# Kernel optimization log

Hardware: AMD Instinct MI355X
Metric: run time of the kernel (lower is better)

Reference implementation:

```python
import jax, jax.numpy as jnp
import numpy as np

TEMPERATURE = 0.1
GAMMA = 0.5
LOSS_WEIGHT = 1.0
N, D = 8192, 64
EPS_COS = 1e-8
EPS_NCE = 1e-6
SQ_EPS = 1e-12  # (1e-6 distance)^2


def setup_inputs() -> dict:
    key = jax.random.key(0)
    k1, k2, k3 = jax.random.split(key, 3)
    features = jax.random.normal(k1, (N, D), dtype=jnp.float32)
    labels = jax.random.randint(k2, (N,), 0, 3, dtype=jnp.int64)
    coords = jax.random.uniform(k3, (N, 3), dtype=jnp.float32)
    return {"features": features, "labels": labels, "coords": coords}


def reference(features, labels, coords):
    # line-point mask (label == 2); pairwise math on the masked subset is
    # expressed as full pairwise + (m_i & m_j) masking, mathematically
    # identical to extract-then-pairwise in the torch original.
    m = labels == 2                       # [N] bool
    mf = m.astype(features.dtype)
    L = jnp.sum(mf)                       # number of line points

    # cosine similarity: normalize then GEMM (== F.cosine_similarity pairwise)
    norm = jnp.maximum(jnp.linalg.norm(features, axis=1, keepdims=True), EPS_COS)
    fn = features / norm
    feat_sim = fn @ fn.T                  # [N, N]

    # squared pairwise coordinate distances (cdist^2), clamped >= 0
    sq_norm = jnp.sum(coords * coords, axis=1)
    sq = sq_norm[:, None] + sq_norm[None, :] - 2.0 * (coords @ coords.T)
    sq = jnp.maximum(sq, 0.0)             # [N, N]

    pair = m[:, None] & m[None, :]
    within = (sq < 1.0) & (sq > SQ_EPS)   # dist < 1.0 and dist > 1e-6
    pos = pair & within
    neg = pair & ~within                  # original neg_mask = ~pos over subset

    posf = pos.astype(feat_sim.dtype)
    negf = neg.astype(feat_sim.dtype)

    exp_sim = jnp.exp(feat_sim / TEMPERATURE)
    sum_exp = jnp.sum(exp_sim * negf, axis=1)
    pos_sum = jnp.sum(exp_sim * posf, axis=1)
    ratio = pos_sum / (sum_exp + pos_sum + EPS_NCE)
    # mean of -log(ratio) over line points only (guard non-line rows)
    per_point = -jnp.log(jnp.where(m, ratio, 1.0))
    info_nce = jnp.sum(per_point * mf) / L

    # continuity: mean over the L x L subset matrix of |(1 - sim) - dist| * pos
    safe_sq = jnp.where(pos, sq, 1.0)     # avoid sqrt(0) NaN grads on masked entries
    coord_dist = jnp.sqrt(safe_sq)
    continuity = jnp.sum(jnp.abs((1.0 - feat_sim) - coord_dist) * posf) / (L * L)

    return (info_nce + GAMMA * continuity) * LOSS_WEIGHT
```

## Files before the change

### kernel.cpp

```cpp
#include <hip/hip_runtime.h>
#include <math.h>


#define NPTS 8192
#define DIM 64
#define TILE 64
#define CHUNKS 32
#define GX 64
#define NCT (GX * CHUNKS)

#define OFF_L 0
#define OFF_IDX 1024
#define OFF_FNT (OFF_IDX + NPTS * 4)
#define OFF_CS (OFF_FNT + DIM * NPTS * 4)
#define OFF_PP (OFF_CS + NPTS * 16)
#define OFF_PN (OFF_PP + CHUNKS * NPTS * 4)
#define OFF_CT (OFF_PN + CHUNKS * NPTS * 4)
#define OFF_DF (OFF_CT + NCT * 4)

__global__ __launch_bounds__(1024) void k_scan(const int* __restrict__ labels,
                                               int* __restrict__ idx,
                                               int* __restrict__ Lout) {
  __shared__ int sc[1024];
  __shared__ int wres[16];
  const int t = threadIdx.x;
  const int base = t * 8;
  int w[8];
#pragma unroll
  for (int j = 0; j < 8; j++) w[j] = labels[base + j];
  int oddz = (w[1] == 0) && (w[3] == 0) && (w[5] == 0) && (w[7] == 0);
  unsigned long long wa = __ballot(!oddz);
  if ((t & 63) == 0) wres[t >> 6] = (wa == 0ull);
  __syncthreads();
  int is64 = 1;
#pragma unroll
  for (int i = 0; i < 16; i++) is64 &= wres[i];

  int bits = 0, cnt = 0;
  if (is64) {
    const long long* l64 = (const long long*)labels;
#pragma unroll
    for (int j = 0; j < 8; j++) {
      bool f = (l64[base + j] == 2ll);
      bits |= ((int)f) << j;
      cnt += (int)f;
    }
  } else {
#pragma unroll
    for (int j = 0; j < 8; j++) {
      bool f = (w[j] == 2);
      bits |= ((int)f) << j;
      cnt += (int)f;
    }
  }
  sc[t] = cnt;
  __syncthreads();
  for (int off = 1; off < 1024; off <<= 1) {
    int v = 0;
    if (t >= off) v = sc[t - off];
    __syncthreads();
    sc[t] += v;
    __syncthreads();
  }
  int pos = sc[t] - cnt;
#pragma unroll
  for (int j = 0; j < 8; j++) {
    if (bits & (1 << j)) idx[pos++] = base + j;
  }
  if (t == 1023) *Lout = sc[1023];
}

__global__ __launch_bounds__(256) void k_gather(const float* __restrict__ feats,
                                                const float* __restrict__ coords,
                                                const int* __restrict__ idx,
                                                const int* __restrict__ Lp,
                                                float* __restrict__ fnT,
                                                float4* __restrict__ cs,
                                                int* __restrict__ diagf) {
  const int L = *Lp;
  const int gw = (int)((blockIdx.x * blockDim.x + threadIdx.x) >> 6);
  const int lane = threadIdx.x & 63;
  if (gw >= L) return;
  const int row = idx[gw];
  float f = feats[row * DIM + lane];
  float ss = f * f;
#pragma unroll
  for (int m = 32; m; m >>= 1) ss += __shfl_xor(ss, m);
  float nrm = fmaxf(sqrtf(ss), 1e-8f);
  fnT[lane * NPTS + gw] = f / nrm;
  if (lane == 0) {
    float c0 = coords[row * 3 + 0];
    float c1 = coords[row * 3 + 1];
    float c2 = coords[row * 3 + 2];
    float p0 = __fmul_rn(c0, c0);
    float p1 = __fmul_rn(c1, c1);
    float p2 = __fmul_rn(c2, c2);
    float s = __fadd_rn(__fadd_rn(p0, p1), p2);
    float g = __fadd_rn(__fadd_rn(p0, p2), p1);
    diagf[gw] = (__fadd_rn(s, -g) > 5e-13f) ? 1 : 0;
    cs[gw] = make_float4(c0, c1, c2, c0 * c0 + c1 * c1 + c2 * c2);
  }
}

__global__ __launch_bounds__(256, 5) void k_pair(const float* __restrict__ fnT,
                                                 const float4* __restrict__ cs,
                                                 const int* __restrict__ Lp,
                                                 const int* __restrict__ diagf,
                                                 float* __restrict__ pp,
                                                 float* __restrict__ pn,
                                                 float* __restrict__ contp) {
  __shared__ float Ak[DIM][TILE];
  __shared__ float Bk[DIM][TILE];
  __shared__ float cred[4];

  const int L = *Lp;
  const int nT = (L + TILE - 1) / TILE;
  const int bx = blockIdx.x, ch = blockIdx.y;
  const int t = threadIdx.x;
  const int tr = t >> 4;
  const int tc = t & 15;
  float cont = 0.f;

  for (int bi = bx; bi < nT; bi += GX) {
    const int rb = bi * TILE;
    __syncthreads();
#pragma unroll
    for (int i = 0; i < 4; i++) {
      int q = t + 256 * i;
      int k = q >> 4;
      int c0 = (q & 15) * 4;
      float4 v = *(const float4*)&fnT[k * NPTS + rb + c0];
      if (rb + c0 + 0 >= L) v.x = 0.f;
      if (rb + c0 + 1 >= L) v.y = 0.f;
      if (rb + c0 + 2 >= L) v.z = 0.f;
      if (rb + c0 + 3 >= L) v.w = 0.f;
      *(float4*)&Ak[k][c0] = v;
    }

    float4 ca[4];
    int dfr[4];
#pragma unroll
    for (int ri = 0; ri < 4; ri++) {
      int ig = rb + tr * 4 + ri;
      ca[ri] = cs[ig];
      dfr[ri] = diagf[ig];
    }

    float pos_r[4] = {0.f, 0.f, 0.f, 0.f};
    float neg_r[4] = {0.f, 0.f, 0.f, 0.f};

    for (int jt = ch; jt < nT; jt += CHUNKS) {
      const int cb = jt * TILE;
      __syncthreads();
#pragma unroll
      for (int i = 0; i < 4; i++) {
        int q = t + 256 * i;
        int k = q >> 4;
        int c0 = (q & 15) * 4;
        float4 v = *(const float4*)&fnT[k * NPTS + cb + c0];
        if (cb + c0 + 0 >= L) v.x = 0.f;
        if (cb + c0 + 1 >= L) v.y = 0.f;
        if (cb + c0 + 2 >= L) v.z = 0.f;
        if (cb + c0 + 3 >= L) v.w = 0.f;
        *(float4*)&Bk[k][c0] = v;
      }
      __syncthreads();

      float acc[4][4];
#pragma unroll
      for (int ri = 0; ri < 4; ri++)
#pragma unroll
        for (int ci = 0; ci < 4; ci++) acc[ri][ci] = 0.f;

#pragma unroll 8
      for (int k = 0; k < DIM; k++) {
        float4 a = *(const float4*)&Ak[k][tr * 4];
        float4 b = *(const float4*)&Bk[k][tc * 4];
        float av[4] = {a.x, a.y, a.z, a.w};
        float bv[4] = {b.x, b.y, b.z, b.w};
#pragma unroll
        for (int ri = 0; ri < 4; ri++)
#pragma unroll
          for (int ci = 0; ci < 4; ci++) acc[ri][ci] += av[ri] * bv[ci];
      }

#pragma unroll
      for (int ci = 0; ci < 4; ci++) {
        int jg = cb + tc * 4 + ci;
        float4 cbv = cs[jg];
        bool jv = (jg < L);
#pragma unroll
        for (int ri = 0; ri < 4; ri++) {
          int ig = rb + tr * 4 + ri;
          bool valid = jv && (ig < L);
          float sim = acc[ri][ci];
          float4 cav = ca[ri];
          float d3 = cav.x * cbv.x + cav.y * cbv.y + cav.z * cbv.z;
          float sq = fmaxf(cav.w + cbv.w - 2.f * d3, 0.f);
          bool within = (sq < 1.0f) && (sq > 1e-12f);
          if (ig == jg) within = (dfr[ri] != 0);
          float e = __expf(sim * 10.f);
          if (valid) {
            if (within) {
              pos_r[ri] += e;
              cont += fabsf(1.f - sim - sqrtf(sq));
            } else {
              neg_r[ri] += e;
            }
          }
        }
      }
    }

#pragma unroll
    for (int ri = 0; ri < 4; ri++) {
      float p = pos_r[ri], n = neg_r[ri];
#pragma unroll
      for (int m = 1; m < 16; m <<= 1) {
        p += __shfl_xor(p, m);
        n += __shfl_xor(n, m);
      }
      if (tc == 0) {
        int ig = rb + tr * 4 + ri;
        pp[ch * NPTS + ig] = p;
        pn[ch * NPTS + ig] = n;
      }
    }
  }

#pragma unroll
  for (int m = 1; m < 64; m <<= 1) cont += __shfl_xor(cont, m);
  if ((t & 63) == 0) cred[t >> 6] = cont;
  __syncthreads();
  if (t == 0) contp[bx * CHUNKS + ch] = cred[0] + cred[1] + cred[2] + cred[3];
}

__global__ __launch_bounds__(1024) void k_final(const float* __restrict__ pp,
                                                const float* __restrict__ pn,
                                                const float* __restrict__ contp,
                                                const int* __restrict__ Lp,
                                                float* __restrict__ out) {
  __shared__ float red[32];
  const int L = *Lp;
  const int t = threadIdx.x;
  float accI = 0.f;
  for (int s = t; s < L; s += 1024) {
    float pos = 0.f, neg = 0.f;
#pragma unroll
    for (int c = 0; c < CHUNKS; c++) {
      pos += pp[c * NPTS + s];
      neg += pn[c * NPTS + s];
    }
    accI += -logf(pos / (neg + pos + 1e-6f));
  }
  float accC = 0.f;
  for (int c = t; c < NCT; c += 1024) accC += contp[c];
#pragma unroll
  for (int m = 1; m < 64; m <<= 1) {
    accI += __shfl_xor(accI, m);
    accC += __shfl_xor(accC, m);
  }
  if ((t & 63) == 0) {
    red[t >> 6] = accI;
    red[16 + (t >> 6)] = accC;
  }
  __syncthreads();
  if (t == 0) {
    float sI = 0.f, sC = 0.f;
#pragma unroll
    for (int w = 0; w < 16; w++) {
      sI += red[w];
      sC += red[16 + w];
    }
    float fL = (float)L;
    out[0] = sI / fL + 0.5f * (sC / (fL * fL));
  }
}

extern "C" void kernel_launch(void* const* d_in, const int* in_sizes, int n_in,
                              void* d_out, int out_size, void* d_ws, size_t ws_size,
                              hipStream_t stream) {
  const float* features = (const float*)d_in[0];
  const int* labels = (const int*)d_in[1];
  const float* coords = (const float*)d_in[2];

  char* ws = (char*)d_ws;
  int* Lp = (int*)(ws + OFF_L);
  int* idx = (int*)(ws + OFF_IDX);
  float* fnT = (float*)(ws + OFF_FNT);
  float4* cs = (float4*)(ws + OFF_CS);
  float* pp = (float*)(ws + OFF_PP);
  float* pn = (float*)(ws + OFF_PN);
  float* contp = (float*)(ws + OFF_CT);
  int* diagf = (int*)(ws + OFF_DF);
  float* out = (float*)d_out;

  k_scan<<<1, 1024, 0, stream>>>(labels, idx, Lp);
  k_gather<<<(NPTS * 64) / 256, 256, 0, stream>>>(features, coords, idx, Lp, fnT, cs, diagf);
  k_pair<<<dim3(GX, CHUNKS), 256, 0, stream>>>(fnT, cs, Lp, diagf, pp, pn, contp);
  k_final<<<1, 1024, 0, stream>>>(pp, pn, contp, Lp, out);
}
```

Before: 53.30 us.

## Use split-bf16 MFMA for pairwise similarity with 128x128 tiles and warp-shuffle scan

The pairwise cosine GEMM moves from scalar FP32 FMAs to bf16 MFMA instructions. Each normalized feature is split into hi and lo bf16 parts and three MFMAs are issued per product to keep near-FP32 accuracy. Work is reorganised into 128x128 tile items spread over a flat persistent grid, with per-column-tile partial sums that the final kernel reduces. The label scan is also rewritten to use wave shuffles instead of a barrier-heavy shared-memory scan. The costs are extra MFMA work for the split precision, a small precision change, and lower occupancy from the larger tiles.

Result: faster. 47.94 us (-10.0%).

```diff
diff --git a/kernel.cpp b/kernel.cpp
--- a/kernel.cpp
+++ b/kernel.cpp
@@ -2,35 +2,41 @@
 #include <math.h>
 
 
+typedef short s16x8 __attribute__((ext_vector_type(8)));
+typedef float f32x4 __attribute__((ext_vector_type(4)));
+
 #define NPTS 8192
 #define DIM 64
-#define TILE 64
-#define CHUNKS 32
-#define GX 64
-#define NCT (GX * CHUNKS)
+#define BT 128
+#define GRID_P 512
+#define PSTRIDE 4096
+#define MAXSLOT 32
 
 #define OFF_L 0
 #define OFF_IDX 1024
-#define OFF_FNT (OFF_IDX + NPTS * 4)
-#define OFF_CS (OFF_FNT + DIM * NPTS * 4)
-#define OFF_PP (OFF_CS + NPTS * 16)
-#define OFF_PN (OFF_PP + CHUNKS * NPTS * 4)
-#define OFF_CT (OFF_PN + CHUNKS * NPTS * 4)
-#define OFF_DF (OFF_CT + NCT * 4)
+#define OFF_FH (OFF_IDX + NPTS * 4)
+#define OFF_FL (OFF_FH + NPTS * DIM * 2)
+#define OFF_CS (OFF_FL + NPTS * DIM * 2)
+#define OFF_DF (OFF_CS + NPTS * 16)
+#define OFF_PP (OFF_DF + NPTS * 4)
+#define OFF_PN (OFF_PP + MAXSLOT * PSTRIDE * 4)
+#define OFF_CT (OFF_PN + MAXSLOT * PSTRIDE * 4)
 
 __global__ __launch_bounds__(1024) void k_scan(const int* __restrict__ labels,
                                                int* __restrict__ idx,
                                                int* __restrict__ Lout) {
-  __shared__ int sc[1024];
   __shared__ int wres[16];
+  __shared__ int wsum[16];
   const int t = threadIdx.x;
+  const int lane = t & 63;
+  const int wid = t >> 6;
   const int base = t * 8;
   int w[8];
 #pragma unroll
   for (int j = 0; j < 8; j++) w[j] = labels[base + j];
   int oddz = (w[1] == 0) && (w[3] == 0) && (w[5] == 0) && (w[7] == 0);
   unsigned long long wa = __ballot(!oddz);
-  if ((t & 63) == 0) wres[t >> 6] = (wa == 0ull);
+  if (lane == 0) wres[wid] = (wa == 0ull);
   __syncthreads();
   int is64 = 1;
 #pragma unroll
@@ -53,41 +59,64 @@
       cnt += (int)f;
     }
   }
-  sc[t] = cnt;
-  __syncthreads();
-  for (int off = 1; off < 1024; off <<= 1) {
-    int v = 0;
-    if (t >= off) v = sc[t - off];
-    __syncthreads();
-    sc[t] += v;
-    __syncthreads();
-  }
-  int pos = sc[t] - cnt;
+  int inc = cnt;
+#pragma unroll
+  for (int m = 1; m < 64; m <<= 1) {
+    int v = __shfl_up(inc, m);
+    if (lane >= m) inc += v;
+  }
+  if (lane == 63) wsum[wid] = inc;
+  __syncthreads();
+  if (t < 16) {
+    int v = wsum[t];
+    int sc = v;
+#pragma unroll
+    for (int m = 1; m < 16; m <<= 1) {
+      int u = __shfl_up(sc, m);
+      if (t >= m) sc += u;
+    }
+    wsum[t] = sc - v;
+    if (t == 15) *Lout = sc;
+  }
+  __syncthreads();
+  int pos = wsum[wid] + inc - cnt;
 #pragma unroll
   for (int j = 0; j < 8; j++) {
     if (bits & (1 << j)) idx[pos++] = base + j;
   }
-  if (t == 1023) *Lout = sc[1023];
 }
 
 __global__ __launch_bounds__(256) void k_gather(const float* __restrict__ feats,
                                                 const float* __restrict__ coords,
                                                 const int* __restrict__ idx,
                                                 const int* __restrict__ Lp,
-                                                float* __restrict__ fnT,
+                                                ushort* __restrict__ fnHi,
+                                                ushort* __restrict__ fnLo,
                                                 float4* __restrict__ cs,
                                                 int* __restrict__ diagf) {
   const int L = *Lp;
   const int gw = (int)((blockIdx.x * blockDim.x + threadIdx.x) >> 6);
   const int lane = threadIdx.x & 63;
-  if (gw >= L) return;
+  if (gw >= L) {
+    fnHi[gw * 64 + lane] = 0;
+    fnLo[gw * 64 + lane] = 0;
+    return;
+  }
   const int row = idx[gw];
   float f = feats[row * DIM + lane];
   float ss = f * f;
 #pragma unroll
   for (int m = 32; m; m >>= 1) ss += __shfl_xor(ss, m);
   float nrm = fmaxf(sqrtf(ss), 1e-8f);
-  fnT[lane * NPTS + gw] = f / nrm;
+  float fn = f / nrm;
+  unsigned int u = __float_as_uint(fn);
+  unsigned int hb = (u + 0x7FFFu + ((u >> 16) & 1u)) >> 16;
+  float hif = __uint_as_float(hb << 16);
+  float lof = fn - hif;
+  unsigned int ul = __float_as_uint(lof);
+  unsigned int lb = (ul + 0x7FFFu + ((ul >> 16) & 1u)) >> 16;
+  fnHi[gw * 64 + lane] = (ushort)hb;
+  fnLo[gw * 64 + lane] = (ushort)lb;
   if (lane == 0) {
     float c0 = coords[row * 3 + 0];
     float c1 = coords[row * 3 + 1];
@@ -102,137 +131,138 @@
   }
 }
 
-__global__ __launch_bounds__(256, 5) void k_pair(const float* __restrict__ fnT,
+__global__ __launch_bounds__(256, 2) void k_pair(const ushort* __restrict__ fnHi,
+                                                 const ushort* __restrict__ fnLo,
                                                  const float4* __restrict__ cs,
                                                  const int* __restrict__ Lp,
                                                  const int* __restrict__ diagf,
                                                  float* __restrict__ pp,
                                                  float* __restrict__ pn,
                                                  float* __restrict__ contp) {
-  __shared__ float Ak[DIM][TILE];
-  __shared__ float Bk[DIM][TILE];
+  __shared__ ushort AB[4][128][72];
   __shared__ float cred[4];
 
   const int L = *Lp;
-  const int nT = (L + TILE - 1) / TILE;
-  const int bx = blockIdx.x, ch = blockIdx.y;
+  const int nT = (L + BT - 1) >> 7;
+  const int nItems = nT * nT;
   const int t = threadIdx.x;
-  const int tr = t >> 4;
-  const int tc = t & 15;
+  const int lane = t & 63, wid = t >> 6;
+  const int m = lane & 15;
+  const int koct = lane >> 4;
   float cont = 0.f;
 
-  for (int bi = bx; bi < nT; bi += GX) {
-    const int rb = bi * TILE;
+  for (int wi = blockIdx.x; wi < nItems; wi += GRID_P) {
+    const int bi = wi / nT;
+    const int jt = wi - bi * nT;
+    const int rb = bi << 7, cb = jt << 7;
+
     __syncthreads();
 #pragma unroll
-    for (int i = 0; i < 4; i++) {
+    for (int i = 0; i < 16; i++) {
       int q = t + 256 * i;
-      int k = q >> 4;
-      int c0 = (q & 15) * 4;
-      float4 v = *(const float4*)&fnT[k * NPTS + rb + c0];
-      if (rb + c0 + 0 >= L) v.x = 0.f;
-      if (rb + c0 + 1 >= L) v.y = 0.f;
-      if (rb + c0 + 2 >= L) v.z = 0.f;
-      if (rb + c0 + 3 >= L) v.w = 0.f;
-      *(float4*)&Ak[k][c0] = v;
-    }
-
-    float4 ca[4];
-    int dfr[4];
-#pragma unroll
-    for (int ri = 0; ri < 4; ri++) {
-      int ig = rb + tr * 4 + ri;
-      ca[ri] = cs[ig];
-      dfr[ri] = diagf[ig];
-    }
-
-    float pos_r[4] = {0.f, 0.f, 0.f, 0.f};
-    float neg_r[4] = {0.f, 0.f, 0.f, 0.f};
-
-    for (int jt = ch; jt < nT; jt += CHUNKS) {
-      const int cb = jt * TILE;
-      __syncthreads();
-#pragma unroll
-      for (int i = 0; i < 4; i++) {
-        int q = t + 256 * i;
-        int k = q >> 4;
-        int c0 = (q & 15) * 4;
-        float4 v = *(const float4*)&fnT[k * NPTS + cb + c0];
-        if (cb + c0 + 0 >= L) v.x = 0.f;
-        if (cb + c0 + 1 >= L) v.y = 0.f;
-        if (cb + c0 + 2 >= L) v.z = 0.f;
-        if (cb + c0 + 3 >= L) v.w = 0.f;
-        *(float4*)&Bk[k][c0] = v;
+      int sel = q >> 10;
+      int row = (q >> 3) & 127;
+      int oct = q & 7;
+      int slot = ((sel < 2) ? rb : cb) + row;
+      const ushort* src = (sel & 1) ? fnLo : fnHi;
+      s16x8 v = *(const s16x8*)&src[slot * 64 + oct * 8];
+      *(s16x8*)&AB[sel][row][oct * 8] = v;
+    }
+    __syncthreads();
+
+    f32x4 acc[2][8];
+#pragma unroll
+    for (int rt = 0; rt < 2; rt++)
+#pragma unroll
+      for (int ct = 0; ct < 8; ct++) acc[rt][ct] = (f32x4){0.f, 0.f, 0.f, 0.f};
+
+#pragma unroll
+    for (int kk = 0; kk < 2; kk++) {
+      const int kof = kk * 32 + koct * 8;
+      s16x8 ah[2], al[2], bh[8], bl[8];
+#pragma unroll
+      for (int rt = 0; rt < 2; rt++) {
+        ah[rt] = *(const s16x8*)&AB[0][wid * 32 + rt * 16 + m][kof];
+        al[rt] = *(const s16x8*)&AB[1][wid * 32 + rt * 16 + m][kof];
       }
-      __syncthreads();
-
-      float acc[4][4];
-#pragma unroll
-      for (int ri = 0; ri < 4; ri++)
-#pragma unroll
-        for (int ci = 0; ci < 4; ci++) acc[ri][ci] = 0.f;
-
-#pragma unroll 8
-      for (int k = 0; k < DIM; k++) {
-        float4 a = *(const float4*)&Ak[k][tr * 4];
-        float4 b = *(const float4*)&Bk[k][tc * 4];
-        float av[4] = {a.x, a.y, a.z, a.w};
-        float bv[4] = {b.x, b.y, b.z, b.w};
-#pragma unroll
-        for (int ri = 0; ri < 4; ri++)
-#pragma unroll
-          for (int ci = 0; ci < 4; ci++) acc[ri][ci] += av[ri] * bv[ci];
+#pragma unroll
+      for (int ct = 0; ct < 8; ct++) {
+        bh[ct] = *(const s16x8*)&AB[2][ct * 16 + m][kof];
+        bl[ct] = *(const s16x8*)&AB[3][ct * 16 + m][kof];
       }
-
-#pragma unroll
-      for (int ci = 0; ci < 4; ci++) {
-        int jg = cb + tc * 4 + ci;
-        float4 cbv = cs[jg];
-        bool jv = (jg < L);
-#pragma unroll
-        for (int ri = 0; ri < 4; ri++) {
-          int ig = rb + tr * 4 + ri;
+#pragma unroll
+      for (int rt = 0; rt < 2; rt++)
+#pragma unroll
+        for (int ct = 0; ct < 8; ct++) {
+          acc[rt][ct] = __builtin_amdgcn_mfma_f32_16x16x32_bf16(ah[rt], bh[ct], acc[rt][ct], 0, 0, 0);
+          acc[rt][ct] = __builtin_amdgcn_mfma_f32_16x16x32_bf16(ah[rt], bl[ct], acc[rt][ct], 0, 0, 0);
+          acc[rt][ct] = __builtin_amdgcn_mfma_f32_16x16x32_bf16(al[rt], bh[ct], acc[rt][ct], 0, 0, 0);
+        }
+    }
+
+    float4 crow[2][4];
+    int dfr[2][4];
+#pragma unroll
+    for (int rt = 0; rt < 2; rt++)
+#pragma unroll
+      for (int rg = 0; rg < 4; rg++) {
+        int ig = rb + wid * 32 + rt * 16 + koct * 4 + rg;
+        crow[rt][rg] = cs[ig];
+        dfr[rt][rg] = diagf[ig];
+      }
+    float pos_r[2][4] = {{0.f, 0.f, 0.f, 0.f}, {0.f, 0.f, 0.f, 0.f}};
+    float neg_r[2][4] = {{0.f, 0.f, 0.f, 0.f}, {0.f, 0.f, 0.f, 0.f}};
+#pragma unroll
+    for (int ct = 0; ct < 8; ct++) {
+      int jg = cb + ct * 16 + m;
+      float4 cbv = cs[jg];
+      bool jv = (jg < L);
+#pragma unroll
+      for (int rt = 0; rt < 2; rt++)
+#pragma unroll
+        for (int rg = 0; rg < 4; rg++) {
+          int ig = rb + wid * 32 + rt * 16 + koct * 4 + rg;
           bool valid = jv && (ig < L);
-          float sim = acc[ri][ci];
-          float4 cav = ca[ri];
+          float sim = acc[rt][ct][rg];
+          float4 cav = crow[rt][rg];
           float d3 = cav.x * cbv.x + cav.y * cbv.y + cav.z * cbv.z;
           float sq = fmaxf(cav.w + cbv.w - 2.f * d3, 0.f);
           bool within = (sq < 1.0f) && (sq > 1e-12f);
-          if (ig == jg) within = (dfr[ri] != 0);
+          if (ig == jg) within = (dfr[rt][rg] != 0);
           float e = __expf(sim * 10.f);
           if (valid) {
             if (within) {
-              pos_r[ri] += e;
+              pos_r[rt][rg] += e;
               cont += fabsf(1.f - sim - sqrtf(sq));
             } else {
-              neg_r[ri] += e;
+              neg_r[rt][rg] += e;
             }
           }
         }
+    }
+#pragma unroll
+    for (int rt = 0; rt < 2; rt++)
+#pragma unroll
+      for (int rg = 0; rg < 4; rg++) {
+        float p = pos_r[rt][rg], n = neg_r[rt][rg];
+#pragma unroll
+        for (int s = 1; s < 16; s <<= 1) {
+          p += __shfl_xor(p, s);
+          n += __shfl_xor(n, s);
+        }
+        if (m == 0) {
+          int ig = rb + wid * 32 + rt * 16 + koct * 4 + rg;
+          pp[jt * PSTRIDE + ig] = p;
+          pn[jt * PSTRIDE + ig] = n;
+        }
       }
-    }
-
-#pragma unroll
-    for (int ri = 0; ri < 4; ri++) {
-      float p = pos_r[ri], n = neg_r[ri];
-#pragma unroll
-      for (int m = 1; m < 16; m <<= 1) {
-        p += __shfl_xor(p, m);
-        n += __shfl_xor(n, m);
-      }
-      if (tc == 0) {
-        int ig = rb + tr * 4 + ri;
-        pp[ch * NPTS + ig] = p;
-        pn[ch * NPTS + ig] = n;
-      }
-    }
-  }
-
-#pragma unroll
-  for (int m = 1; m < 64; m <<= 1) cont += __shfl_xor(cont, m);
-  if ((t & 63) == 0) cred[t >> 6] = cont;
-  __syncthreads();
-  if (t == 0) contp[bx * CHUNKS + ch] = cred[0] + cred[1] + cred[2] + cred[3];
+  }
+
+#pragma unroll
+  for (int s = 1; s < 64; s <<= 1) cont += __shfl_xor(cont, s);
+  if (lane == 0) cred[wid] = cont;
+  __syncthreads();
+  if (t == 0) contp[blockIdx.x] = cred[0] + cred[1] + cred[2] + cred[3];
 }
 
 __global__ __launch_bounds__(1024) void k_final(const float* __restrict__ pp,
@@ -242,19 +272,19 @@
                                                 float* __restrict__ out) {
   __shared__ float red[32];
   const int L = *Lp;
+  const int nslots = (L + BT - 1) >> 7;
   const int t = threadIdx.x;
   float accI = 0.f;
   for (int s = t; s < L; s += 1024) {
     float pos = 0.f, neg = 0.f;
-#pragma unroll
-    for (int c = 0; c < CHUNKS; c++) {
-      pos += pp[c * NPTS + s];
-      neg += pn[c * NPTS + s];
+    for (int c = 0; c < nslots; c++) {
+      pos += pp[c * PSTRIDE + s];
+      neg += pn[c * PSTRIDE + s];
     }
     accI += -logf(pos / (neg + pos + 1e-6f));
   }
   float accC = 0.f;
-  for (int c = t; c < NCT; c += 1024) accC += contp[c];
+  for (int c = t; c < GRID_P; c += 1024) accC += contp[c];
 #pragma unroll
   for (int m = 1; m < 64; m <<= 1) {
     accI += __shfl_xor(accI, m);
@@ -287,16 +317,17 @@
   char* ws = (char*)d_ws;
   int* Lp = (int*)(ws + OFF_L);
   int* idx = (int*)(ws + OFF_IDX);
-  float* fnT = (float*)(ws + OFF_FNT);
+  ushort* fnHi = (ushort*)(ws + OFF_FH);
+  ushort* fnLo = (ushort*)(ws + OFF_FL);
   float4* cs = (float4*)(ws + OFF_CS);
+  int* diagf = (int*)(ws + OFF_DF);
   float* pp = (float*)(ws + OFF_PP);
   float* pn = (float*)(ws + OFF_PN);
   float* contp = (float*)(ws + OFF_CT);
-  int* diagf = (int*)(ws + OFF_DF);
   float* out = (float*)d_out;
 
   k_scan<<<1, 1024, 0, stream>>>(labels, idx, Lp);
-  k_gather<<<(NPTS * 64) / 256, 256, 0, stream>>>(features, coords, idx, Lp, fnT, cs, diagf);
-  k_pair<<<dim3(GX, CHUNKS), 256, 0, stream>>>(fnT, cs, Lp, diagf, pp, pn, contp);
+  k_gather<<<(NPTS * 64) / 256, 256, 0, stream>>>(features, coords, idx, Lp, fnHi, fnLo, cs, diagf);
+  k_pair<<<GRID_P, 256, 0, stream>>>(fnHi, fnLo, cs, Lp, diagf, pp, pn, contp);
   k_final<<<1, 1024, 0, stream>>>(pp, pn, contp, Lp, out);
 }
```
